# Kernel optimization log

Measured on AMD Instinct MI355X. Metric: run time of the kernel, lower is better.

The kernel has to match this reference:

```python
import jax, jax.numpy as jnp
import numpy as np
from jax import lax

B, L, H = 32, 4096, 512  # batch, v_len (encoder frames), hidden_dim


def setup_inputs() -> dict:
    key = jax.random.key(0)
    ks = jax.random.split(key, 9)
    return {
        "query": jax.random.normal(ks[0], (B, 1, H), dtype=jnp.float32),
        "value": jax.random.normal(ks[1], (B, L, H), dtype=jnp.float32),
        "last_attn": jax.random.uniform(ks[2], (B, L), dtype=jnp.float32),
        # conv1d: in_channels=1, out_channels=H, kernel_size=3
        "conv_w": jax.random.normal(ks[3], (H, 1, 3), dtype=jnp.float32) * 0.1,
        "conv_b": jax.random.normal(ks[4], (H,), dtype=jnp.float32) * 0.1,
        "Wq": jax.random.normal(ks[5], (H, H), dtype=jnp.float32) / np.sqrt(H),
        "Wv": jax.random.normal(ks[6], (H, H), dtype=jnp.float32) / np.sqrt(H),
        "Ws": jax.random.normal(ks[7], (H,), dtype=jnp.float32) / np.sqrt(H),  # score_proj weight (1,H) flattened
        "bs": jnp.zeros((), dtype=jnp.float32),  # score_proj bias
        "bias": jax.random.uniform(ks[8], (H,), minval=-0.1, maxval=0.1, dtype=jnp.float32),
    }


def reference(query, value, last_attn, conv_w, conv_b, Wq, Wv, Ws, bs, bias):
    # conv1d over previous alignment: (B,1,L) -> (B,H,L), then transpose to (B,L,H)
    conv_attn = lax.conv_general_dilated(
        last_attn[:, None, :], conv_w, window_strides=(1,), padding=[(1, 1)],
        dimension_numbers=("NCH", "OIH", "NCH"))
    conv_attn = conv_attn.transpose(0, 2, 1) + conv_b[None, None, :]  # (B,L,H)

    q = jnp.einsum("bqh,oh->bqo", query, Wq)   # (B,1,H), broadcasts over L
    v = jnp.einsum("blh,oh->blo", value, Wv)   # (B,L,H)
    e = jnp.tanh(q + v + conv_attn + bias)     # (B,L,H)
    score = jnp.einsum("blh,h->bl", e, Ws) + bs  # (B,L)

    # smoothing=True branch: sigmoid + sum-normalize
    score = jax.nn.sigmoid(score)
    attn = score / jnp.sum(score, axis=-1, keepdims=True)  # (B,L)

    context = jnp.einsum("bl,blh->bh", attn, value)  # (B,H)
    out = jnp.concatenate([context, query[:, 0, :]], axis=1)  # (B,2H)
    return out, attn
```

## Files before the change

### kernel.cpp

```cpp
#include <hip/hip_runtime.h>
#include <hip/hip_bf16.h>
#include <math.h>

#define BB 32
#define LL 4096
#define HH 512
#define TM 32

typedef __attribute__((ext_vector_type(8))) short short8;
typedef __attribute__((ext_vector_type(8))) unsigned short u16x8;
typedef __attribute__((ext_vector_type(4))) float f32x4;

__device__ __forceinline__ unsigned short f2bf(float f) {
  __hip_bfloat16 h = __float2bfloat16(f);
  unsigned short u;
  __builtin_memcpy(&u, &h, 2);
  return u;
}
__device__ __forceinline__ float bf2f(unsigned short u) {
  unsigned int x = ((unsigned int)u) << 16;
  float f;
  __builtin_memcpy(&f, &x, 4);
  return f;
}
__device__ __forceinline__ float fast_tanh(float x) {
  float e = __expf(2.f * x);
  return 1.f - 2.f / (e + 1.f);
}

__global__ __launch_bounds__(256) void prep_kernel(
    const float* __restrict__ query, const float* __restrict__ Wq,
    const float* __restrict__ bias, const float* __restrict__ conv_b,
    const float* __restrict__ Wv, float* __restrict__ base,
    unsigned short* __restrict__ wvf, float* __restrict__ ctx) {
  const int bid = blockIdx.x;
  if (bid < 64) {
    const int b = bid >> 1;
    const int o = ((bid & 1) << 8) + threadIdx.x;
    __shared__ float qrow[HH];
    for (int i = threadIdx.x; i < HH; i += 256) qrow[i] = query[b * HH + i];
    __syncthreads();
    const float* wq = Wq + (size_t)o * HH;
    float acc = 0.f;
    for (int h = 0; h < HH; h += 4) {
      float4 w = *(const float4*)(wq + h);
      acc += w.x * qrow[h] + w.y * qrow[h + 1] + w.z * qrow[h + 2] + w.w * qrow[h + 3];
    }
    base[b * HH + o] = acc + bias[o] + conv_b[o];
    ctx[b * HH + o] = 0.f;
  } else {
    const int chunk = (bid - 64) * 256 + threadIdx.x;
    const int l = chunk & 63;
    const int kk = (chunk >> 6) & 15;
    const int nb = chunk >> 10;
    const int row = nb * 16 + (l & 15);
    const int colf = kk * 32 + (l >> 4) * 8;
    const float* src = Wv + (size_t)row * HH + colf;
    u16x8 v;
    #pragma unroll
    for (int j = 0; j < 8; ++j) v[j] = f2bf(src[j]);
    *(u16x8*)(wvf + (size_t)chunk * 8) = v;
  }
}

__global__ __launch_bounds__(512, 6) void main_kernel(
    const float* __restrict__ value, const float* __restrict__ last_attn,
    const float* __restrict__ conv_w, const unsigned short* __restrict__ wvf,
    const float* __restrict__ Ws, const float* __restrict__ bs,
    const float* __restrict__ base, float* __restrict__ ctx,
    float* __restrict__ attn) {
  const int b = blockIdx.y;
  const int l0 = blockIdx.x * TM;
  const int tid = threadIdx.x;
  const int w = tid >> 6;
  const int lane = tid & 63;
  const int g = lane >> 4;
  const int r16 = lane & 15;

  __shared__ __align__(16) unsigned short A[TM * HH];
  __shared__ float la_s[TM + 2];
  __shared__ float scorered[8][TM];
  __shared__ float srow[TM];
  __shared__ float ctxsum[HH];

  char* Ab = (char*)A;

  const float* vsrc = value + (size_t)(b * LL + l0) * HH;
  #pragma unroll
  for (int i = 0; i < 4; ++i) {
    const int c = tid + i * 512;
    const int row = c >> 6;
    const int cb = c & 63;
    const float4* s4 = (const float4*)(vsrc + (size_t)row * HH + cb * 8);
    float4 lo = s4[0], hi = s4[1];
    u16x8 v;
    v[0] = f2bf(lo.x); v[1] = f2bf(lo.y); v[2] = f2bf(lo.z); v[3] = f2bf(lo.w);
    v[4] = f2bf(hi.x); v[5] = f2bf(hi.y); v[6] = f2bf(hi.z); v[7] = f2bf(hi.w);
    const int off = row * 1024 + ((cb * 16) ^ ((row & 7) << 4));
    *(u16x8*)(Ab + off) = v;
  }
  ctxsum[tid] = 0.f;
  if (tid < TM + 2) {
    int l = l0 - 1 + tid;
    la_s[tid] = (l >= 0 && l < LL) ? last_attn[b * LL + l] : 0.f;
  }
  __syncthreads();

  f32x4 acc[2][4] = {};
  const int kk0 = (blockIdx.x + (blockIdx.y << 2)) & 15;
  #pragma unroll 2
  for (int i = 0; i < 16; ++i) {
    const int kk = (kk0 + i) & 15;
    const int co = kk * 64 + g * 16;
    const int row0 = r16, row1 = 16 + r16;
    short8 a0 = *(const short8*)(Ab + row0 * 1024 + (co ^ ((row0 & 7) << 4)));
    short8 a1 = *(const short8*)(Ab + row1 * 1024 + (co ^ ((row1 & 7) << 4)));
    #pragma unroll
    for (int n = 0; n < 4; ++n) {
      short8 bf = *(const short8*)(wvf + ((size_t)((w * 4 + n) * 16 + kk) * 64 + lane) * 8);
      acc[0][n] = __builtin_amdgcn_mfma_f32_16x16x32_bf16(a0, bf, acc[0][n], 0, 0, 0);
      acc[1][n] = __builtin_amdgcn_mfma_f32_16x16x32_bf16(a1, bf, acc[1][n], 0, 0, 0);
    }
  }

  float basev[4], wsv[4], cw0[4], cw1[4], cw2[4];
  #pragma unroll
  for (int n = 0; n < 4; ++n) {
    const int col = w * 64 + n * 16 + r16;
    basev[n] = base[b * HH + col];
    wsv[n] = Ws[col];
    cw0[n] = conv_w[col * 3 + 0];
    cw1[n] = conv_w[col * 3 + 1];
    cw2[n] = conv_w[col * 3 + 2];
  }
  #pragma unroll
  for (int m = 0; m < 2; ++m) {
    #pragma unroll
    for (int j = 0; j < 4; ++j) {
      const int row = m * 16 + g * 4 + j;
      const float lam = la_s[row], laz = la_s[row + 1], lap = la_s[row + 2];
      float sum = 0.f;
      #pragma unroll
      for (int n = 0; n < 4; ++n) {
        float e = acc[m][n][j] + basev[n] + cw0[n] * lam + cw1[n] * laz + cw2[n] * lap;
        sum += fast_tanh(e) * wsv[n];
      }
      sum += __shfl_xor(sum, 1, 64);
      sum += __shfl_xor(sum, 2, 64);
      sum += __shfl_xor(sum, 4, 64);
      sum += __shfl_xor(sum, 8, 64);
      if (r16 == 0) scorered[w][row] = sum;
    }
  }
  __syncthreads();
  if (tid < TM) {
    float sc = bs[0];
    #pragma unroll
    for (int ww = 0; ww < 8; ++ww) sc += scorered[ww][tid];
    float s = 1.f / (1.f + __expf(-sc));
    srow[tid] = s;
    attn[b * LL + l0 + tid] = s;
  }
  __syncthreads();

  {
    float cs[8];
    #pragma unroll
    for (int k = 0; k < 8; ++k) cs[k] = 0.f;
    #pragma unroll
    for (int i = 0; i < 4; ++i) {
      const int row = w * 4 + i;
      const int off = row * 1024 + ((lane * 16) ^ ((row & 7) << 4));
      u16x8 v = *(const u16x8*)(Ab + off);
      const float s = srow[row];
      #pragma unroll
      for (int k = 0; k < 8; ++k) cs[k] += s * bf2f(v[k]);
    }
    #pragma unroll
    for (int k = 0; k < 8; ++k) atomicAdd(&ctxsum[lane * 8 + k], cs[k]);
  }
  __syncthreads();
  atomicAdd(&ctx[b * HH + tid], ctxsum[tid]);
}

__global__ __launch_bounds__(512) void finalize_kernel(
    const float* __restrict__ query, const float* __restrict__ ctx,
    float* __restrict__ out, float* __restrict__ attn) {
  const int b = blockIdx.x;
  const int tid = threadIdx.x;
  __shared__ float red[8];
  float s = 0.f;
  for (int l = tid; l < LL; l += 512) s += attn[b * LL + l];
  #pragma unroll
  for (int off = 32; off > 0; off >>= 1) s += __shfl_xor(s, off, 64);
  if ((tid & 63) == 0) red[tid >> 6] = s;
  __syncthreads();
  float S = 0.f;
  #pragma unroll
  for (int i = 0; i < 8; ++i) S += red[i];
  const float inv = 1.f / S;
  out[b * 2 * HH + tid] = ctx[b * HH + tid] * inv;
  out[b * 2 * HH + HH + tid] = query[b * HH + tid];
  for (int l = tid; l < LL; l += 512) attn[b * LL + l] *= inv;
}

extern "C" void kernel_launch(void* const* d_in, const int* in_sizes, int n_in,
                              void* d_out, int out_size, void* d_ws, size_t ws_size,
                              hipStream_t stream) {
  const float* query     = (const float*)d_in[0];
  const float* value     = (const float*)d_in[1];
  const float* last_attn = (const float*)d_in[2];
  const float* conv_w    = (const float*)d_in[3];
  const float* conv_b    = (const float*)d_in[4];
  const float* Wq        = (const float*)d_in[5];
  const float* Wv        = (const float*)d_in[6];
  const float* Ws        = (const float*)d_in[7];
  const float* bs        = (const float*)d_in[8];
  const float* bias      = (const float*)d_in[9];

  float* out  = (float*)d_out;
  float* attn = out + BB * 2 * HH;
  float* base = (float*)d_ws;
  float* ctx  = base + BB * HH;
  unsigned short* wvf = (unsigned short*)(ctx + BB * HH);

  prep_kernel<<<192, 256, 0, stream>>>(query, Wq, bias, conv_b, Wv, base, wvf, ctx);
  dim3 grid(LL / TM, BB);
  main_kernel<<<grid, 512, 0, stream>>>(value, last_attn, conv_w, wvf, Ws, bs,
                                        base, ctx, attn);
  finalize_kernel<<<BB, 512, 0, stream>>>(query, ctx, out, attn);
}
```

Before: 220.8 us.

## Make main kernel persistent over four tiles with register-prefetched value loads

Each block now processes four L-tiles instead of one, cutting the grid from 128x32 to 32x32 blocks. While one tile's MFMA GEMM and score epilogue run, the next tile's value rows and last_attn are prefetched into registers, then converted to bf16 and stored into LDS. Context partial sums stay in registers across tiles, so the shared and global atomics happen once per block instead of once per tile. In exchange it uses more registers (occupancy hint lowered from 6 to 4), adds extra barriers, drops the rotated k-start used to spread Wv reads, and leaves fewer blocks to fill the GPU.

```diff
diff --git a/kernel.cpp b/kernel.cpp
--- a/kernel.cpp
+++ b/kernel.cpp
@@ -6,6 +6,7 @@
 #define LL 4096
 #define HH 512
 #define TM 32
+#define NT 4
 
 typedef __attribute__((ext_vector_type(8))) short short8;
 typedef __attribute__((ext_vector_type(8))) unsigned short u16x8;
@@ -63,14 +64,14 @@
   }
 }
 
-__global__ __launch_bounds__(512, 6) void main_kernel(
+__global__ __launch_bounds__(512, 4) void main_kernel(
     const float* __restrict__ value, const float* __restrict__ last_attn,
     const float* __restrict__ conv_w, const unsigned short* __restrict__ wvf,
     const float* __restrict__ Ws, const float* __restrict__ bs,
     const float* __restrict__ base, float* __restrict__ ctx,
     float* __restrict__ attn) {
   const int b = blockIdx.y;
-  const int l0 = blockIdx.x * TM;
+  const int gx = blockIdx.x;
   const int tid = threadIdx.x;
   const int w = tid >> 6;
   const int lane = tid & 63;
@@ -85,88 +86,117 @@
 
   char* Ab = (char*)A;
 
-  const float* vsrc = value + (size_t)(b * LL + l0) * HH;
-  #pragma unroll
-  for (int i = 0; i < 4; ++i) {
-    const int c = tid + i * 512;
-    const int row = c >> 6;
-    const int cb = c & 63;
-    const float4* s4 = (const float4*)(vsrc + (size_t)row * HH + cb * 8);
-    float4 lo = s4[0], hi = s4[1];
-    u16x8 v;
-    v[0] = f2bf(lo.x); v[1] = f2bf(lo.y); v[2] = f2bf(lo.z); v[3] = f2bf(lo.w);
-    v[4] = f2bf(hi.x); v[5] = f2bf(hi.y); v[6] = f2bf(hi.z); v[7] = f2bf(hi.w);
-    const int off = row * 1024 + ((cb * 16) ^ ((row & 7) << 4));
-    *(u16x8*)(Ab + off) = v;
-  }
-  ctxsum[tid] = 0.f;
-  if (tid < TM + 2) {
-    int l = l0 - 1 + tid;
-    la_s[tid] = (l >= 0 && l < LL) ? last_attn[b * LL + l] : 0.f;
-  }
-  __syncthreads();
-
-  f32x4 acc[2][4] = {};
-  const int kk0 = (blockIdx.x + (blockIdx.y << 2)) & 15;
-  #pragma unroll 2
-  for (int i = 0; i < 16; ++i) {
-    const int kk = (kk0 + i) & 15;
-    const int co = kk * 64 + g * 16;
-    const int row0 = r16, row1 = 16 + r16;
-    short8 a0 = *(const short8*)(Ab + row0 * 1024 + (co ^ ((row0 & 7) << 4)));
-    short8 a1 = *(const short8*)(Ab + row1 * 1024 + (co ^ ((row1 & 7) << 4)));
-    #pragma unroll
-    for (int n = 0; n < 4; ++n) {
-      short8 bf = *(const short8*)(wvf + ((size_t)((w * 4 + n) * 16 + kk) * 64 + lane) * 8);
-      acc[0][n] = __builtin_amdgcn_mfma_f32_16x16x32_bf16(a0, bf, acc[0][n], 0, 0, 0);
-      acc[1][n] = __builtin_amdgcn_mfma_f32_16x16x32_bf16(a1, bf, acc[1][n], 0, 0, 0);
-    }
-  }
-
-  float basev[4], wsv[4], cw0[4], cw1[4], cw2[4];
+  float basev[4], wsv[4], cw0v[4], cw1v[4], cw2v[4];
   #pragma unroll
   for (int n = 0; n < 4; ++n) {
     const int col = w * 64 + n * 16 + r16;
     basev[n] = base[b * HH + col];
-    wsv[n] = Ws[col];
-    cw0[n] = conv_w[col * 3 + 0];
-    cw1[n] = conv_w[col * 3 + 1];
-    cw2[n] = conv_w[col * 3 + 2];
-  }
-  #pragma unroll
-  for (int m = 0; m < 2; ++m) {
-    #pragma unroll
-    for (int j = 0; j < 4; ++j) {
-      const int row = m * 16 + g * 4 + j;
-      const float lam = la_s[row], laz = la_s[row + 1], lap = la_s[row + 2];
-      float sum = 0.f;
+    wsv[n]  = Ws[col];
+    cw0v[n] = conv_w[col * 3 + 0];
+    cw1v[n] = conv_w[col * 3 + 1];
+    cw2v[n] = conv_w[col * 3 + 2];
+  }
+  float cacc[8];
+  #pragma unroll
+  for (int k = 0; k < 8; ++k) cacc[k] = 0.f;
+  ctxsum[tid] = 0.f;
+
+  float4 st[8];
+  float lan = 0.f;
+  {
+    const float* vs = value + ((size_t)b * LL + gx * TM) * HH;
+    #pragma unroll
+    for (int i = 0; i < 4; ++i) {
+      const int c = tid + i * 512;
+      const float* p = vs + (size_t)(c >> 6) * HH + (c & 63) * 8;
+      st[2 * i]     = *(const float4*)p;
+      st[2 * i + 1] = *(const float4*)(p + 4);
+    }
+    if (tid < TM + 2) {
+      int l = gx * TM - 1 + tid;
+      lan = (l >= 0 && l < LL) ? last_attn[b * LL + l] : 0.f;
+    }
+  }
+  #pragma unroll
+  for (int i = 0; i < 4; ++i) {
+    const int c = tid + i * 512;
+    const int row = c >> 6, cb = c & 63;
+    u16x8 v;
+    v[0] = f2bf(st[2*i].x);   v[1] = f2bf(st[2*i].y);
+    v[2] = f2bf(st[2*i].z);   v[3] = f2bf(st[2*i].w);
+    v[4] = f2bf(st[2*i+1].x); v[5] = f2bf(st[2*i+1].y);
+    v[6] = f2bf(st[2*i+1].z); v[7] = f2bf(st[2*i+1].w);
+    *(u16x8*)(Ab + row * 1024 + ((cb * 16) ^ ((row & 7) << 4))) = v;
+  }
+  if (tid < TM + 2) la_s[tid] = lan;
+  __syncthreads();
+
+  const short8* bp = (const short8*)wvf + (size_t)(w * 4) * 16 * 64;
+
+  for (int t = 0; t < NT; ++t) {
+    const int l0 = (gx + 32 * t) * TM;
+
+    f32x4 acc[2][4] = {};
+    #pragma unroll 2
+    for (int kk = 0; kk < 16; ++kk) {
+      const int co = kk * 64 + g * 16;
+      const int row1 = 16 + r16;
+      short8 a0 = *(const short8*)(Ab + r16  * 1024 + (co ^ ((r16  & 7) << 4)));
+      short8 a1 = *(const short8*)(Ab + row1 * 1024 + (co ^ ((row1 & 7) << 4)));
       #pragma unroll
       for (int n = 0; n < 4; ++n) {
-        float e = acc[m][n][j] + basev[n] + cw0[n] * lam + cw1[n] * laz + cw2[n] * lap;
-        sum += fast_tanh(e) * wsv[n];
-      }
-      sum += __shfl_xor(sum, 1, 64);
-      sum += __shfl_xor(sum, 2, 64);
-      sum += __shfl_xor(sum, 4, 64);
-      sum += __shfl_xor(sum, 8, 64);
-      if (r16 == 0) scorered[w][row] = sum;
-    }
-  }
-  __syncthreads();
-  if (tid < TM) {
-    float sc = bs[0];
-    #pragma unroll
-    for (int ww = 0; ww < 8; ++ww) sc += scorered[ww][tid];
-    float s = 1.f / (1.f + __expf(-sc));
-    srow[tid] = s;
-    attn[b * LL + l0 + tid] = s;
-  }
-  __syncthreads();
-
-  {
-    float cs[8];
-    #pragma unroll
-    for (int k = 0; k < 8; ++k) cs[k] = 0.f;
+        short8 bf = bp[(n * 16 + kk) * 64 + lane];
+        acc[0][n] = __builtin_amdgcn_mfma_f32_16x16x32_bf16(a0, bf, acc[0][n], 0, 0, 0);
+        acc[1][n] = __builtin_amdgcn_mfma_f32_16x16x32_bf16(a1, bf, acc[1][n], 0, 0, 0);
+      }
+    }
+
+    const int tn = t + 1;
+    if (tn < NT) {
+      const float* vs = value + ((size_t)b * LL + (gx + 32 * tn) * TM) * HH;
+      #pragma unroll
+      for (int i = 0; i < 4; ++i) {
+        const int c = tid + i * 512;
+        const float* p = vs + (size_t)(c >> 6) * HH + (c & 63) * 8;
+        st[2 * i]     = *(const float4*)p;
+        st[2 * i + 1] = *(const float4*)(p + 4);
+      }
+      if (tid < TM + 2) {
+        int l = (gx + 32 * tn) * TM - 1 + tid;
+        lan = (l < LL) ? last_attn[b * LL + l] : 0.f;
+      }
+    }
+
+    #pragma unroll
+    for (int m = 0; m < 2; ++m) {
+      #pragma unroll
+      for (int j = 0; j < 4; ++j) {
+        const int row = m * 16 + g * 4 + j;
+        const float lam = la_s[row], laz = la_s[row + 1], lap = la_s[row + 2];
+        float sum = 0.f;
+        #pragma unroll
+        for (int n = 0; n < 4; ++n) {
+          float e = acc[m][n][j] + basev[n] + cw0v[n] * lam + cw1v[n] * laz + cw2v[n] * lap;
+          sum += fast_tanh(e) * wsv[n];
+        }
+        sum += __shfl_xor(sum, 1, 64);
+        sum += __shfl_xor(sum, 2, 64);
+        sum += __shfl_xor(sum, 4, 64);
+        sum += __shfl_xor(sum, 8, 64);
+        if (r16 == 0) scorered[w][row] = sum;
+      }
+    }
+    __syncthreads();
+    if (tid < TM) {
+      float sc = bs[0];
+      #pragma unroll
+      for (int ww = 0; ww < 8; ++ww) sc += scorered[ww][tid];
+      float s = 1.f / (1.f + __expf(-sc));
+      srow[tid] = s;
+      attn[b * LL + l0 + tid] = s;
+    }
+    __syncthreads();
+
     #pragma unroll
     for (int i = 0; i < 4; ++i) {
       const int row = w * 4 + i;
@@ -174,11 +204,29 @@
       u16x8 v = *(const u16x8*)(Ab + off);
       const float s = srow[row];
       #pragma unroll
-      for (int k = 0; k < 8; ++k) cs[k] += s * bf2f(v[k]);
-    }
-    #pragma unroll
-    for (int k = 0; k < 8; ++k) atomicAdd(&ctxsum[lane * 8 + k], cs[k]);
-  }
+      for (int k = 0; k < 8; ++k) cacc[k] += s * bf2f(v[k]);
+    }
+    __syncthreads();
+
+    if (tn < NT) {
+      #pragma unroll
+      for (int i = 0; i < 4; ++i) {
+        const int c = tid + i * 512;
+        const int row = c >> 6, cb = c & 63;
+        u16x8 v;
+        v[0] = f2bf(st[2*i].x);   v[1] = f2bf(st[2*i].y);
+        v[2] = f2bf(st[2*i].z);   v[3] = f2bf(st[2*i].w);
+        v[4] = f2bf(st[2*i+1].x); v[5] = f2bf(st[2*i+1].y);
+        v[6] = f2bf(st[2*i+1].z); v[7] = f2bf(st[2*i+1].w);
+        *(u16x8*)(Ab + row * 1024 + ((cb * 16) ^ ((row & 7) << 4))) = v;
+      }
+      if (tid < TM + 2) la_s[tid] = lan;
+      __syncthreads();
+    }
+  }
+
+  #pragma unroll
+  for (int k = 0; k < 8; ++k) atomicAdd(&ctxsum[lane * 8 + k], cacc[k]);
   __syncthreads();
   atomicAdd(&ctx[b * HH + tid], ctxsum[tid]);
 }
@@ -225,7 +273,7 @@
   unsigned short* wvf = (unsigned short*)(ctx + BB * HH);
 
   prep_kernel<<<192, 256, 0, stream>>>(query, Wq, bias, conv_b, Wv, base, wvf, ctx);
-  dim3 grid(LL / TM, BB);
+  dim3 grid(32, BB);
   main_kernel<<<grid, 512, 0, stream>>>(value, last_attn, conv_w, wvf, Ws, bs,
                                         base, ctx, attn);
   finalize_kernel<<<BB, 512, 0, stream>>>(query, ctx, out, attn);
```

Measured after the change: 249.6 us. +13.1%, slower.
